# Kernel tuning notes

Measured on AMD Instinct MI355X. Metric: run time of the kernel, lower is better.

The kernel has to match this reference:

```python
import jax, jax.numpy as jnp
import numpy as np

C, N, E = 256, 256, 2048          # subgraphs, nodes/subgraph, edges/subgraph
F_IN, NHID, DDI = 128, 128, 256
K1, K2, K3 = 128, 64, 32          # top-k sizes for pooling_ratio=0.5
P, B = 16, 16                     # DAG hierarchy: P parents x B leaf children
GN = C + P + 1                    # global DAG nodes (leaves + parents + root)
GE = 8192                         # global pos/neg edge count


def setup_inputs():
    key = jax.random.key(0)
    ks = jax.random.split(key, 16)
    inp = {
        "x": jax.random.normal(ks[0], (C, N, F_IN), jnp.float32),
        "edge_index": jax.random.randint(ks[1], (C, 2, E), 0, N),
        "edge_weight": jax.random.uniform(ks[2], (C, E), dtype=jnp.float32),
        "global_edge_index": jax.random.randint(ks[3], (2, GE), 0, GN),
        "neg_edge_index": jax.random.randint(ks[4], (2, GE), 0, GN),
    }
    names = [("W1", F_IN, NHID), ("Wp1", NHID, 1), ("W2", NHID, NHID),
             ("Wp2", NHID, 1), ("W3", NHID, NHID), ("Wp3", NHID, 1),
             ("Wg", 6 * NHID, DDI), ("Wl1", DDI, DDI), ("Wl2", DDI, DDI)]
    for i, (nm, fi, fo) in enumerate(names):
        inp[nm] = jax.random.normal(ks[5 + i], (fi, fo), jnp.float32) / np.sqrt(fi)
        inp["b" + nm[1:]] = jnp.zeros((fo,), jnp.float32)
    return inp


def gcn(x, ei, ew, W, b):
    """PyG GCNConv with self-loops: D^-1/2 (A+I) D^-1/2 X W + b."""
    n = x.shape[0]
    h = x @ W
    row, col = ei[0], ei[1]
    deg = 1.0 + jax.ops.segment_sum(ew, col, num_segments=n)
    dis = jax.lax.rsqrt(deg)
    norm = dis[row] * ew * dis[col]                       # [E]
    agg = jax.ops.segment_sum(norm[:, None] * h[row], col, num_segments=n)
    return agg + h / deg[:, None] + b


def sag_pool(x, ei, ew, Ws, bs, k):
    """SAGPooling: GCN score, per-graph top-k, gate by tanh(score), edge filter."""
    n = x.shape[0]
    score = gcn(x, ei, ew, Ws, bs)[:, 0]
    vals, perm = jax.lax.top_k(score, k)
    x_new = x[perm] * jnp.tanh(vals)[:, None]
    newid = jnp.full((n,), -1, jnp.int32).at[perm].set(jnp.arange(k, dtype=jnp.int32))
    r, c = newid[ei[0]], newid[ei[1]]
    keep = (r >= 0) & (c >= 0)
    ei_new = jnp.where(keep, jnp.stack([r, c]), 0)        # dropped edges -> node 0
    ew_new = jnp.where(keep, ew, 0.0)                     # with zero weight
    return x_new, ei_new, ew_new


def _subgraph(x, ei, ew, W1, b1, Wp1, bp1, W2, b2, Wp2, bp2, W3, b3, Wp3, bp3):
    x = jax.nn.relu(gcn(x, ei, ew, W1, b1))
    x, ei, ew = sag_pool(x, ei, ew, Wp1, bp1, K1)
    x1 = jnp.concatenate([x.max(0), x.mean(0)])           # gmp||gap, batch all-zero
    x = jax.nn.relu(gcn(x, ei, ew, W2, b2))
    x, ei, ew = sag_pool(x, ei, ew, Wp2, bp2, K2)
    x2 = jnp.concatenate([x.max(0), x.mean(0)])
    x = jax.nn.relu(gcn(x, ei, ew, W3, b3))
    x, ei, ew = sag_pool(x, ei, ew, Wp3, bp3, K3)
    x3 = jnp.concatenate([x.max(0), x.mean(0)])
    return jnp.concatenate([x1, x2, x3])                  # [6*NHID]


def reference(x, edge_index, edge_weight, global_edge_index, neg_edge_index,
              W1, b1, Wp1, bp1, W2, b2, Wp2, bp2, W3, b3, Wp3, bp3,
              Wg, bg, Wl1, bl1, Wl2, bl2):
    # per-class subgraph pipeline, vmapped over the C subgraphs
    leaf = jax.vmap(_subgraph, in_axes=(0, 0, 0) + (None,) * 12)(
        x, edge_index, edge_weight,
        W1, b1, Wp1, bp1, W2, b2, Wp2, bp2, W3, b3, Wp3, bp3)   # [C, 6*NHID]
    # Get_Fs: mean-aggregate children features up the DAG (fixed 2-level + root)
    parent = leaf.reshape(P, B, -1).mean(axis=1)                # [P, 6*NHID]
    root = parent.mean(axis=0, keepdims=True)                   # [1, 6*NHID]
    gfeat = jnp.concatenate([leaf, parent, root], axis=0)       # [GN, 6*NHID]
    # global GCN (unit edge weights)
    gx = jax.nn.relu(gcn(gfeat, global_edge_index,
                         jnp.ones((GE,), gfeat.dtype), Wg, bg)) # [GN, DDI]
    class_embedding = gx[:C]
    # feature_split + lin1/lin2 + dot-product scores
    pos_s = gx[global_edge_index[0]] @ Wl1 + bl1
    pos_t = gx[global_edge_index[1]] @ Wl2 + bl2
    neg_s = gx[neg_edge_index[0]] @ Wl1 + bl1
    neg_t = gx[neg_edge_index[1]] @ Wl2 + bl2
    pos = jnp.sum(pos_s * pos_t, axis=1)
    neg = jnp.sum(neg_s * neg_t, axis=1)
    # BCEWithLogits: targets 1 for pos, 0 for neg
    loss = jnp.mean(jax.nn.softplus(-pos)) + jnp.mean(jax.nn.softplus(neg))
    return class_embedding, loss
```

## Files before the change

### kernel.cpp

```cpp
#include <hip/hip_runtime.h>
#include <math.h>

#define NT 1024
#define EDGES 2048
#define SENT 0xFFFF

struct SmemA {
  float xbuf[256 * 128];
  unsigned short rc[EDGES];
  float ewl[EDGES];
  unsigned short csr_row[EDGES];
  float csr_coef[EDGES];
  float degs[256];
  float diss[256];
  int   csr_off[257];
  int   csr_cnt[256];
  float hsv[256];
  float scorev[256];
  float vals[128];
  short perm[128];
  signed char newid[256];
};

__device__ __forceinline__ float4* xvec(float* xb, int row, int c4) {
  return reinterpret_cast<float4*>(xb + (row << 7) + ((c4 ^ (row & 7)) << 2));
}
__device__ __forceinline__ int xidx(int row, int col) {
  return (row << 7) + ((((col >> 2) ^ (row & 7)) << 2) | (col & 3));
}

template<int NN, int K, bool FIRST, bool REMAP>
__device__ __forceinline__ void run_stage(
    SmemA& sm,
    const float* __restrict__ xg,
    const int* __restrict__ eic,
    const float* __restrict__ ewc,
    const float* __restrict__ W,
    const float* __restrict__ b,
    const float* __restrict__ Wp,
    const float* __restrict__ bp,
    float& lmax, float& lmean)
{
  constexpr int NPT  = NN / 64;
  constexpr int Q    = NN / 64;
  constexpr int SEG  = NT / NN;
  constexpr int LEN  = NN / SEG;
  constexpr int LOG  = (NN == 256) ? 8 : (NN == 128 ? 7 : 6);
  const int tid  = threadIdx.x;
  const int lane = tid & 63;
  const int fbase = __builtin_amdgcn_readfirstlane((tid >> 6) << 3);
  const int c4b   = fbase >> 2;

  if (FIRST) {
    if (tid < NN) { sm.degs[tid] = 1.0f; sm.csr_cnt[tid] = 0; }
    __syncthreads();
    const float4* xg4 = reinterpret_cast<const float4*>(xg);
    for (int i = tid; i < 256 * 32; i += NT) {
      const float4 v = xg4[i];
      *xvec(sm.xbuf, i >> 5, i & 31) = v;
    }
    for (int e = tid; e < EDGES; e += NT) {
      const int row = eic[e], col = eic[EDGES + e];
      const float w = ewc[e];
      sm.rc[e]  = (unsigned short)((row << 8) | col);
      sm.ewl[e] = w;
      atomicAdd(&sm.degs[col], w);
      atomicAdd(&sm.csr_cnt[col], 1);
    }
    __syncthreads();
  }

  if (tid < NN) sm.diss[tid] = rsqrtf(sm.degs[tid]);
  if (tid < 64) {
    int c[Q], pre[Q];
    int tot = 0;
#pragma unroll
    for (int i = 0; i < Q; i++) { c[i] = sm.csr_cnt[tid * Q + i]; pre[i] = tot; tot += c[i]; }
    int inc = tot;
#pragma unroll
    for (int d = 1; d < 64; d <<= 1) {
      const int o = __shfl_up(inc, d, 64);
      if (tid >= d) inc += o;
    }
    const int base = inc - tot;
    if (tid == 0) sm.csr_off[0] = 0;
#pragma unroll
    for (int i = 0; i < Q; i++) {
      sm.csr_off[tid * Q + i + 1] = base + pre[i] + c[i];
      sm.csr_cnt[tid * Q + i] = 0;
    }
  }
  __syncthreads();

  if (tid < NN) { sm.hsv[tid] = 0.0f; sm.scorev[tid] = 0.0f; }
  for (int e = tid; e < EDGES; e += NT) {
    const unsigned short r = sm.rc[e];
    if (FIRST || r != SENT) {
      const int row = r >> 8, col = r & 255;
      const int p = atomicAdd(&sm.csr_cnt[col], 1);
      const int s = sm.csr_off[col] + p;
      sm.csr_row[s]  = (unsigned short)row;
      sm.csr_coef[s] = sm.diss[row] * sm.ewl[e];
    }
  }
  __syncthreads();

  float acc[NPT][8];
#pragma unroll
  for (int i = 0; i < NPT; i++)
#pragma unroll
    for (int j = 0; j < 8; j++) acc[i][j] = 0.0f;

#pragma unroll 4
  for (int k4 = 0; k4 < 32; k4++) {
    float4 xv[NPT];
#pragma unroll
    for (int i = 0; i < NPT; i++) xv[i] = *xvec(sm.xbuf, lane + (i << 6), k4);
#pragma unroll
    for (int kk = 0; kk < 4; kk++) {
      const float* wr = W + (((k4 << 2) + kk) << 7) + fbase;
      const float4 wa = *reinterpret_cast<const float4*>(wr);
      const float4 wb = *reinterpret_cast<const float4*>(wr + 4);
      const float wv[8] = {wa.x, wa.y, wa.z, wa.w, wb.x, wb.y, wb.z, wb.w};
#pragma unroll
      for (int i = 0; i < NPT; i++) {
        const float xs = (kk == 0) ? xv[i].x : (kk == 1) ? xv[i].y : (kk == 2) ? xv[i].z : xv[i].w;
#pragma unroll
        for (int j = 0; j < 8; j++) acc[i][j] = fmaf(xs, wv[j], acc[i][j]);
      }
    }
  }
  __syncthreads();

#pragma unroll
  for (int i = 0; i < NPT; i++) {
    const int v = lane + (i << 6);
    *xvec(sm.xbuf, v, c4b)     = make_float4(acc[i][0], acc[i][1], acc[i][2], acc[i][3]);
    *xvec(sm.xbuf, v, c4b + 1) = make_float4(acc[i][4], acc[i][5], acc[i][6], acc[i][7]);
  }
  __syncthreads();

  {
    const float4 ba = *reinterpret_cast<const float4*>(b + fbase);
    const float4 bb = *reinterpret_cast<const float4*>(b + fbase + 4);
    const float bv[8] = {ba.x, ba.y, ba.z, ba.w, bb.x, bb.y, bb.z, bb.w};
    const float4 wa = *reinterpret_cast<const float4*>(Wp + fbase);
    const float4 wb = *reinterpret_cast<const float4*>(Wp + fbase + 4);
    const float wv[8] = {wa.x, wa.y, wa.z, wa.w, wb.x, wb.y, wb.z, wb.w};
#pragma unroll
    for (int i = 0; i < NPT; i++) {
      const int v = lane + (i << 6);
      const int beg = sm.csr_off[v], end = sm.csr_off[v + 1];
      float ag[8] = {0.f, 0.f, 0.f, 0.f, 0.f, 0.f, 0.f, 0.f};
      float4 plo = make_float4(0.f, 0.f, 0.f, 0.f), phi = plo;
      float cf_nxt = 0.0f;
      if (beg < end) {
        const int r0 = sm.csr_row[beg];
        cf_nxt = sm.csr_coef[beg];
        plo = *xvec(sm.xbuf, r0, c4b);
        phi = *xvec(sm.xbuf, r0, c4b + 1);
      }
      for (int s = beg; s < end; ++s) {
        const float4 lo = plo, hi = phi;
        const float cf = cf_nxt;
        if (s + 1 < end) {
          const int rn = sm.csr_row[s + 1];
          cf_nxt = sm.csr_coef[s + 1];
          plo = *xvec(sm.xbuf, rn, c4b);
          phi = *xvec(sm.xbuf, rn, c4b + 1);
        }
        ag[0] = fmaf(cf, lo.x, ag[0]); ag[1] = fmaf(cf, lo.y, ag[1]);
        ag[2] = fmaf(cf, lo.z, ag[2]); ag[3] = fmaf(cf, lo.w, ag[3]);
        ag[4] = fmaf(cf, hi.x, ag[4]); ag[5] = fmaf(cf, hi.y, ag[5]);
        ag[6] = fmaf(cf, hi.z, ag[6]); ag[7] = fmaf(cf, hi.w, ag[7]);
      }
      const float dv = sm.diss[v];
      const float invd = 1.0f / sm.degs[v];
      float part = 0.0f;
#pragma unroll
      for (int j = 0; j < 8; j++) {
        acc[i][j] = fmaxf(fmaf(ag[j], dv, fmaf(acc[i][j], invd, bv[j])), 0.0f);
        part = fmaf(acc[i][j], wv[j], part);
      }
      atomicAdd(&sm.hsv[v], part);
    }
  }
  __syncthreads();

#pragma unroll
  for (int i = 0; i < NPT; i++) {
    const int v = lane + (i << 6);
    *xvec(sm.xbuf, v, c4b)     = make_float4(acc[i][0], acc[i][1], acc[i][2], acc[i][3]);
    *xvec(sm.xbuf, v, c4b + 1) = make_float4(acc[i][4], acc[i][5], acc[i][6], acc[i][7]);
  }
  for (int e = tid; e < EDGES; e += NT) {
    const unsigned short r = sm.rc[e];
    if (FIRST || r != SENT) {
      const int row = r >> 8, col = r & 255;
      atomicAdd(&sm.scorev[col], sm.diss[row] * sm.ewl[e] * sm.hsv[row]);
    }
  }
  __syncthreads();
  if (tid < NN) {
    sm.scorev[tid] = sm.scorev[tid] * sm.diss[tid] + sm.hsv[tid] / sm.degs[tid] + bp[0];
    sm.csr_cnt[tid] = 0;
  }
  __syncthreads();

  {
    const int node = tid & (NN - 1);
    const int seg  = tid >> LOG;
    const float sv = sm.scorev[node];
    int part = 0;
    const int u0 = seg * LEN;
#pragma unroll 4
    for (int u = u0; u < u0 + LEN; u++) {
      const float su = sm.scorev[u];
      part += (su > sv) || (su == sv && u < node);
    }
    if (part) atomicAdd(&sm.csr_cnt[node], part);
  }
  __syncthreads();
  if (tid < NN) {
    const int rank = sm.csr_cnt[tid];
    if (rank < K) { sm.perm[rank] = (short)tid; sm.vals[rank] = sm.scorev[tid]; sm.newid[tid] = (signed char)rank; }
    else sm.newid[tid] = -1;
    if (tid < K) { sm.degs[tid] = 1.0f; sm.csr_cnt[tid] = 0; }
  }
  __syncthreads();

  {
    constexpr int TPR = NT / K;
    constexpr int C4  = 32 / TPR;
    const int drow = tid / TPR;
    const int cc   = (tid % TPR) * C4;
    const int src  = sm.perm[drow];
    const float g  = tanhf(sm.vals[drow]);
    float4 tmp[C4];
#pragma unroll
    for (int j = 0; j < C4; j++) tmp[j] = *xvec(sm.xbuf, src, cc + j);
    __syncthreads();
#pragma unroll
    for (int j = 0; j < C4; j++) {
      tmp[j].x *= g; tmp[j].y *= g; tmp[j].z *= g; tmp[j].w *= g;
      *xvec(sm.xbuf, drow, cc + j) = tmp[j];
    }
  }
  __syncthreads();

  if (tid < 128) {
    float mx = -INFINITY, sv = 0.0f;
    for (int i = 0; i < K; i++) {
      const float v = sm.xbuf[xidx(i, tid)];
      mx = fmaxf(mx, v); sv += v;
    }
    lmax = mx;
    lmean = sv * (1.0f / K);
  }
  if (REMAP) {
    for (int e = tid; e < EDGES; e += NT) {
      const unsigned short r = sm.rc[e];
      if (FIRST || r != SENT) {
        const int r2 = sm.newid[r >> 8];
        const int c2 = sm.newid[r & 255];
        if (r2 < 0 || c2 < 0) sm.rc[e] = SENT;
        else {
          sm.rc[e] = (unsigned short)((r2 << 8) | c2);
          atomicAdd(&sm.degs[c2], sm.ewl[e]);
          atomicAdd(&sm.csr_cnt[c2], 1);
        }
      }
    }
  }
  __syncthreads();
}

__global__ __launch_bounds__(NT)
void stageA_kernel(const float* __restrict__ x0,
                   const int* __restrict__ ei, const float* __restrict__ ew,
                   const int* __restrict__ gei,
                   const float* __restrict__ W1, const float* __restrict__ b1,
                   const float* __restrict__ Wp1, const float* __restrict__ bp1,
                   const float* __restrict__ W2, const float* __restrict__ b2,
                   const float* __restrict__ Wp2, const float* __restrict__ bp2,
                   const float* __restrict__ W3, const float* __restrict__ b3,
                   const float* __restrict__ Wp3, const float* __restrict__ bp3,
                   const float* __restrict__ Wg, float* __restrict__ hG,
                   float* __restrict__ degG, int* __restrict__ goff,
                   int* __restrict__ gcsr_row, float* __restrict__ gcsr_coef,
                   float* __restrict__ lacc, int* __restrict__ lctr,
                   int* __restrict__ pctr)
{
  __shared__ SmemA sm;
  const int c = blockIdx.x;
  const int tid = threadIdx.x;

  if (c == 256) {
    int* cnt = (int*)sm.xbuf;
    int* off = cnt + 320;
    int* fc  = off + 321;
    for (int i = tid; i < 320; i += NT) cnt[i] = 0;
    if (tid < 288) fc[tid] = 0;
    __syncthreads();
    for (int e = tid; e < 8192; e += NT) atomicAdd(&cnt[gei[8192 + e]], 1);
    __syncthreads();
    if (tid < 64) {
      int cc[5], pre[5];
      int tot = 0;
#pragma unroll
      for (int i = 0; i < 5; i++) { cc[i] = cnt[tid * 5 + i]; pre[i] = tot; tot += cc[i]; }
      int inc = tot;
#pragma unroll
      for (int d = 1; d < 64; d <<= 1) {
        const int o = __shfl_up(inc, d, 64);
        if (tid >= d) inc += o;
      }
      const int base = inc - tot;
      if (tid == 0) off[0] = 0;
#pragma unroll
      for (int i = 0; i < 5; i++) off[tid * 5 + i + 1] = base + pre[i] + cc[i];
    }
    if (tid < 273) degG[tid] = 1.0f + (float)cnt[tid];
    __syncthreads();
    for (int e = tid; e < 8192; e += NT) {
      const int col = gei[8192 + e], row = gei[e];
      const int p = atomicAdd(&fc[col], 1);
      const int s = off[col] + p;
      gcsr_row[s]  = row;
      gcsr_coef[s] = rsqrtf(1.0f + (float)cnt[row]);
    }
    if (tid < 274) goff[tid] = off[tid];
    if (tid == 0) { *lacc = 0.0f; *lctr = 0; }

    if (tid == 0) {
      while (__hip_atomic_load(pctr, __ATOMIC_ACQUIRE, __HIP_MEMORY_SCOPE_AGENT) < 256)
        __builtin_amdgcn_s_sleep(8);
    }
    __syncthreads();
    __threadfence();

    float* racc = sm.hsv;
    if (tid < 256) racc[tid] = 0.0f;
    __syncthreads();
    for (int w = tid; w < 16 * 256; w += NT) {
      const int p = w >> 8, f = w & 255;
      float s = 0.f;
#pragma unroll 4
      for (int b2 = 0; b2 < 16; b2++) s += hG[(size_t)(p * 16 + b2) * 256 + f];
      hG[(size_t)(256 + p) * 256 + f] = s * (1.0f / 16.0f);
      atomicAdd(&racc[f], s * (1.0f / 256.0f));
    }
    __syncthreads();
    if (tid < 256) hG[(size_t)272 * 256 + tid] = racc[tid];
    return;
  }

  const int* eic = ei + (size_t)c * 2 * EDGES;
  const float* ewc = ew + (size_t)c * EDGES;
  const float* xgc = x0 + (size_t)c * 256 * 128;
  float l0 = 0.f, l1 = 0.f, l2 = 0.f, l3 = 0.f, l4 = 0.f, l5 = 0.f;
  run_stage<256, 128, true,  true >(sm, xgc, eic, ewc, W1, b1, Wp1, bp1, l0, l1);
  run_stage<128,  64, false, true >(sm, nullptr, nullptr, nullptr, W2, b2, Wp2, bp2, l2, l3);
  run_stage< 64,  32, false, false>(sm, nullptr, nullptr, nullptr, W3, b3, Wp3, bp3, l4, l5);

  float* leafbuf = sm.csr_coef;
  float* hGacc   = sm.degs;
  if (tid < 256) {
    if (tid < 128) {
      leafbuf[tid]       = l0; leafbuf[128 + tid] = l1;
      leafbuf[256 + tid] = l2; leafbuf[384 + tid] = l3;
      leafbuf[512 + tid] = l4; leafbuf[640 + tid] = l5;
    }
    hGacc[tid] = 0.0f;
  }
  __syncthreads();
  {
    const int f = tid & 255, q = tid >> 8;
    const float* wgq = Wg + (size_t)(q * 192) * 256 + f;
    const float* lb  = leafbuf + q * 192;
    float p0 = 0.f, p1 = 0.f, p2 = 0.f, p3 = 0.f;
    for (int i = 0; i < 192; i += 4) {
      p0 = fmaf(lb[i],     wgq[(size_t)i * 256],       p0);
      p1 = fmaf(lb[i + 1], wgq[(size_t)(i + 1) * 256], p1);
      p2 = fmaf(lb[i + 2], wgq[(size_t)(i + 2) * 256], p2);
      p3 = fmaf(lb[i + 3], wgq[(size_t)(i + 3) * 256], p3);
    }
    atomicAdd(&hGacc[f], (p0 + p1) + (p2 + p3));
  }
  __syncthreads();
  if (tid < 256) hG[(size_t)c * 256 + tid] = hGacc[tid];

  __syncthreads();
  if (tid == 0) {
    __threadfence();
    __hip_atomic_fetch_add(pctr, 1, __ATOMIC_RELEASE, __HIP_MEMORY_SCOPE_AGENT);
  }
}

__global__ __launch_bounds__(NT)
void gaggemb_k(const float* __restrict__ hG, const float* __restrict__ degG,
               const int* __restrict__ goff, const int* __restrict__ gcsr_row,
               const float* __restrict__ gcsr_coef, const float* __restrict__ bg,
               const float* __restrict__ Wl1, const float* __restrict__ bl1,
               const float* __restrict__ Wl2, const float* __restrict__ bl2,
               float* __restrict__ out_ce, float* __restrict__ A,
               float* __restrict__ B) {
  __shared__ float pacc[1024];
  __shared__ float pacc2[1024];
  __shared__ float gxr[256];
  const int v = blockIdx.x, tid = threadIdx.x;
  const int f = tid & 255, q = tid >> 8;
  const int beg = goff[v], end = goff[v + 1];
  float s = 0.f;
  for (int i = beg + q; i < end; i += 4)
    s = fmaf(gcsr_coef[i], hG[(size_t)gcsr_row[i] * 256 + f], s);
  pacc[tid] = s;
  __syncthreads();
  if (tid < 256) {
    const float dg = degG[v];
    float val = (pacc[tid] + pacc[256 + tid] + pacc[512 + tid] + pacc[768 + tid]) * rsqrtf(dg)
              + hG[(size_t)v * 256 + tid] / dg + bg[tid];
    val = fmaxf(val, 0.0f);
    gxr[tid] = val;
    if (v < 256) out_ce[(size_t)v * 256 + tid] = val;
  }
  __syncthreads();
  {
    const int k0 = q << 6;
    float a = 0.f, b2 = 0.f;
    for (int k = k0; k < k0 + 64; k++) {
      const float g = gxr[k];
      a  = fmaf(g, Wl1[(size_t)k * 256 + f], a);
      b2 = fmaf(g, Wl2[(size_t)k * 256 + f], b2);
    }
    pacc[tid] = a; pacc2[tid] = b2;
  }
  __syncthreads();
  if (tid < 256) {
    A[(size_t)v * 256 + tid] = pacc[tid] + pacc[256 + tid] + pacc[512 + tid] + pacc[768 + tid] + bl1[tid];
    B[(size_t)v * 256 + tid] = pacc2[tid] + pacc2[256 + tid] + pacc2[512 + tid] + pacc2[768 + tid] + bl2[tid];
  }
}

__global__ __launch_bounds__(256)
void loss_k(const float* __restrict__ A, const float* __restrict__ B,
            const int* __restrict__ gei, const int* __restrict__ nei,
            float* __restrict__ acc, int* __restrict__ lctr,
            float* __restrict__ out) {
  const int gw = (blockIdx.x * blockDim.x + threadIdx.x) >> 6;
  const int lane = threadIdx.x & 63;
  float lsum = 0.0f;
  for (int idx = gw; idx < 16384; idx += 512) {
    const bool ispos = idx < 8192;
    const int e = ispos ? idx : idx - 8192;
    const int* ia = ispos ? gei : nei;
    const int s = ia[e], t = ia[8192 + e];
    float p = 0.0f;
#pragma unroll
    for (int j = 0; j < 4; j++)
      p += A[(size_t)s * 256 + lane + 64 * j] * B[(size_t)t * 256 + lane + 64 * j];
#pragma unroll
    for (int off = 32; off; off >>= 1) p += __shfl_xor(p, off, 64);
    const float z = ispos ? -p : p;
    lsum += fmaxf(z, 0.0f) + log1pf(expf(-fabsf(z)));
  }
  if (lane == 0) atomicAdd(acc, lsum);
  __syncthreads();
  if (threadIdx.x == 0) {
    __threadfence();
    const int old = atomicAdd(lctr, 1);
    if (old == (int)gridDim.x - 1) {
      const float tot = atomicAdd(acc, 0.0f);
      out[65536] = tot * (1.0f / 8192.0f);
    }
  }
}

extern "C" void kernel_launch(void* const* d_in, const int* in_sizes, int n_in,
                              void* d_out, int out_size, void* d_ws, size_t ws_size,
                              hipStream_t stream) {
  const float* x   = (const float*)d_in[0];
  const int*   ei  = (const int*)d_in[1];
  const float* ew  = (const float*)d_in[2];
  const int*   gei = (const int*)d_in[3];
  const int*   nei = (const int*)d_in[4];
  const float* W1  = (const float*)d_in[5];
  const float* b1  = (const float*)d_in[6];
  const float* Wp1 = (const float*)d_in[7];
  const float* bp1 = (const float*)d_in[8];
  const float* W2  = (const float*)d_in[9];
  const float* b2  = (const float*)d_in[10];
  const float* Wp2 = (const float*)d_in[11];
  const float* bp2 = (const float*)d_in[12];
  const float* W3  = (const float*)d_in[13];
  const float* b3  = (const float*)d_in[14];
  const float* Wp3 = (const float*)d_in[15];
  const float* bp3 = (const float*)d_in[16];
  const float* Wg  = (const float*)d_in[17];
  const float* bg  = (const float*)d_in[18];
  const float* Wl1 = (const float*)d_in[19];
  const float* bl1 = (const float*)d_in[20];
  const float* Wl2 = (const float*)d_in[21];
  const float* bl2 = (const float*)d_in[22];

  float* ws       = (float*)d_ws;
  float* hG       = ws;
  float* degG     = hG + 273 * 256;
  float* Aemb     = degG + 288;
  float* Bemb     = Aemb + 273 * 256;
  float* lacc     = Bemb + 273 * 256;
  int*   lctr     = (int*)(lacc + 1);
  int*   pctr     = lctr + 1;
  int*   goff     = pctr + 1;
  int*   gcsr_row = goff + 288;
  float* gcsr_coef= (float*)(gcsr_row + 8192);
  float* out      = (float*)d_out;

  hipMemsetAsync(pctr, 0, sizeof(int), stream);
  stageA_kernel<<<257, NT, 0, stream>>>(x, ei, ew, gei, W1, b1, Wp1, bp1,
                                        W2, b2, Wp2, bp2, W3, b3, Wp3, bp3,
                                        Wg, hG, degG, goff, gcsr_row, gcsr_coef,
                                        lacc, lctr, pctr);
  gaggemb_k<<<273, NT, 0, stream>>>(hG, degG, goff, gcsr_row, gcsr_coef, bg,
                                    Wl1, bl1, Wl2, bl2, out, Aemb, Bemb);
  loss_k<<<128, 256, 0, stream>>>(Aemb, Bemb, gei, nei, lacc, lctr, out);
}
```

Baseline: 207.3 us.

## Split DAG prep into own kernel and fuse global GCN with loss via grid barrier

Removes the spin-waiting extra block from the subgraph kernel. Global CSR build and parent/root averaging move into a separate 17-block prep kernel, which spreads the parent reduction over 16 blocks and drops the host memset. The global aggregation/embedding kernel and the loss kernel are fused behind a software grid barrier across all 273 blocks, which relies on those blocks being co-resident. One __syncthreads after the per-subgraph CSR fill is also removed; this risks a race if later code reads the CSR before every thread has finished writing it.

```diff
diff --git a/kernel.cpp b/kernel.cpp
--- a/kernel.cpp
+++ b/kernel.cpp
@@ -103,7 +103,6 @@
       sm.csr_coef[s] = sm.diss[row] * sm.ewl[e];
     }
   }
-  __syncthreads();
 
   float acc[NPT][8];
 #pragma unroll
@@ -278,83 +277,18 @@
 __global__ __launch_bounds__(NT)
 void stageA_kernel(const float* __restrict__ x0,
                    const int* __restrict__ ei, const float* __restrict__ ew,
-                   const int* __restrict__ gei,
                    const float* __restrict__ W1, const float* __restrict__ b1,
                    const float* __restrict__ Wp1, const float* __restrict__ bp1,
                    const float* __restrict__ W2, const float* __restrict__ b2,
                    const float* __restrict__ Wp2, const float* __restrict__ bp2,
                    const float* __restrict__ W3, const float* __restrict__ b3,
                    const float* __restrict__ Wp3, const float* __restrict__ bp3,
-                   const float* __restrict__ Wg, float* __restrict__ hG,
-                   float* __restrict__ degG, int* __restrict__ goff,
-                   int* __restrict__ gcsr_row, float* __restrict__ gcsr_coef,
-                   float* __restrict__ lacc, int* __restrict__ lctr,
-                   int* __restrict__ pctr)
+                   const float* __restrict__ Wg, float* __restrict__ hG)
 {
   __shared__ SmemA sm;
   const int c = blockIdx.x;
   const int tid = threadIdx.x;
-
-  if (c == 256) {
-    int* cnt = (int*)sm.xbuf;
-    int* off = cnt + 320;
-    int* fc  = off + 321;
-    for (int i = tid; i < 320; i += NT) cnt[i] = 0;
-    if (tid < 288) fc[tid] = 0;
-    __syncthreads();
-    for (int e = tid; e < 8192; e += NT) atomicAdd(&cnt[gei[8192 + e]], 1);
-    __syncthreads();
-    if (tid < 64) {
-      int cc[5], pre[5];
-      int tot = 0;
-#pragma unroll
-      for (int i = 0; i < 5; i++) { cc[i] = cnt[tid * 5 + i]; pre[i] = tot; tot += cc[i]; }
-      int inc = tot;
-#pragma unroll
-      for (int d = 1; d < 64; d <<= 1) {
-        const int o = __shfl_up(inc, d, 64);
-        if (tid >= d) inc += o;
-      }
-      const int base = inc - tot;
-      if (tid == 0) off[0] = 0;
-#pragma unroll
-      for (int i = 0; i < 5; i++) off[tid * 5 + i + 1] = base + pre[i] + cc[i];
-    }
-    if (tid < 273) degG[tid] = 1.0f + (float)cnt[tid];
-    __syncthreads();
-    for (int e = tid; e < 8192; e += NT) {
-      const int col = gei[8192 + e], row = gei[e];
-      const int p = atomicAdd(&fc[col], 1);
-      const int s = off[col] + p;
-      gcsr_row[s]  = row;
-      gcsr_coef[s] = rsqrtf(1.0f + (float)cnt[row]);
-    }
-    if (tid < 274) goff[tid] = off[tid];
-    if (tid == 0) { *lacc = 0.0f; *lctr = 0; }
-
-    if (tid == 0) {
-      while (__hip_atomic_load(pctr, __ATOMIC_ACQUIRE, __HIP_MEMORY_SCOPE_AGENT) < 256)
-        __builtin_amdgcn_s_sleep(8);
-    }
-    __syncthreads();
-    __threadfence();
-
-    float* racc = sm.hsv;
-    if (tid < 256) racc[tid] = 0.0f;
-    __syncthreads();
-    for (int w = tid; w < 16 * 256; w += NT) {
-      const int p = w >> 8, f = w & 255;
-      float s = 0.f;
-#pragma unroll 4
-      for (int b2 = 0; b2 < 16; b2++) s += hG[(size_t)(p * 16 + b2) * 256 + f];
-      hG[(size_t)(256 + p) * 256 + f] = s * (1.0f / 16.0f);
-      atomicAdd(&racc[f], s * (1.0f / 256.0f));
-    }
-    __syncthreads();
-    if (tid < 256) hG[(size_t)272 * 256 + tid] = racc[tid];
-    return;
-  }
-
+  if (c == 0 && tid < 256) hG[(size_t)272 * 256 + tid] = 0.0f;
   const int* eic = ei + (size_t)c * 2 * EDGES;
   const float* ewc = ew + (size_t)c * EDGES;
   const float* xgc = x0 + (size_t)c * 256 * 128;
@@ -389,32 +323,90 @@
   }
   __syncthreads();
   if (tid < 256) hG[(size_t)c * 256 + tid] = hGacc[tid];
-
-  __syncthreads();
-  if (tid == 0) {
-    __threadfence();
-    __hip_atomic_fetch_add(pctr, 1, __ATOMIC_RELEASE, __HIP_MEMORY_SCOPE_AGENT);
-  }
 }
 
 __global__ __launch_bounds__(NT)
-void gaggemb_k(const float* __restrict__ hG, const float* __restrict__ degG,
-               const int* __restrict__ goff, const int* __restrict__ gcsr_row,
-               const float* __restrict__ gcsr_coef, const float* __restrict__ bg,
-               const float* __restrict__ Wl1, const float* __restrict__ bl1,
-               const float* __restrict__ Wl2, const float* __restrict__ bl2,
-               float* __restrict__ out_ce, float* __restrict__ A,
-               float* __restrict__ B) {
+void prep_k(float* __restrict__ hG, const int* __restrict__ gei,
+            float* __restrict__ degG, int* __restrict__ goff,
+            int* __restrict__ gcsr_row, float* __restrict__ gcsr_coef,
+            float* __restrict__ lacc, int* __restrict__ lctr,
+            int* __restrict__ arrive) {
+  const int tid = threadIdx.x;
+  if (blockIdx.x == 16) {
+    __shared__ int cnt[320];
+    __shared__ int off[321];
+    __shared__ int fc[288];
+    for (int i = tid; i < 320; i += NT) cnt[i] = 0;
+    if (tid < 288) fc[tid] = 0;
+    __syncthreads();
+    for (int e = tid; e < 8192; e += NT) atomicAdd(&cnt[gei[8192 + e]], 1);
+    __syncthreads();
+    if (tid < 64) {
+      int cc[5], pre[5];
+      int tot = 0;
+#pragma unroll
+      for (int i = 0; i < 5; i++) { cc[i] = cnt[tid * 5 + i]; pre[i] = tot; tot += cc[i]; }
+      int inc = tot;
+#pragma unroll
+      for (int d = 1; d < 64; d <<= 1) {
+        const int o = __shfl_up(inc, d, 64);
+        if (tid >= d) inc += o;
+      }
+      const int base = inc - tot;
+      if (tid == 0) off[0] = 0;
+#pragma unroll
+      for (int i = 0; i < 5; i++) off[tid * 5 + i + 1] = base + pre[i] + cc[i];
+    }
+    if (tid < 273) degG[tid] = 1.0f + (float)cnt[tid];
+    __syncthreads();
+    for (int e = tid; e < 8192; e += NT) {
+      const int col = gei[8192 + e], row = gei[e];
+      const int p = atomicAdd(&fc[col], 1);
+      const int s = off[col] + p;
+      gcsr_row[s]  = row;
+      gcsr_coef[s] = rsqrtf(1.0f + (float)cnt[row]);
+    }
+    if (tid < 274) goff[tid] = off[tid];
+    if (tid == 0) { *lacc = 0.0f; *lctr = 0; *arrive = 0; }
+    return;
+  }
+  __shared__ float pr[1024];
+  const int p = blockIdx.x;
+  const int f = tid & 255, q = tid >> 8;
+  float s = 0.f;
+  for (int b2 = q; b2 < 16; b2 += 4) s += hG[(size_t)(p * 16 + b2) * 256 + f];
+  pr[tid] = s;
+  __syncthreads();
+  if (tid < 256) {
+    const float sv = (pr[tid] + pr[256 + tid] + pr[512 + tid] + pr[768 + tid]) * (1.0f / 16.0f);
+    hG[(size_t)(256 + p) * 256 + tid] = sv;
+    atomicAdd(&hG[(size_t)272 * 256 + tid], sv * (1.0f / 16.0f));
+  }
+}
+
+__global__ __launch_bounds__(NT)
+void gagg_loss_k(const float* __restrict__ hG, const float* __restrict__ degG,
+                 const int* __restrict__ goff, const int* __restrict__ gcsr_row,
+                 const float* __restrict__ gcsr_coef, const float* __restrict__ bg,
+                 const float* __restrict__ Wl1, const float* __restrict__ bl1,
+                 const float* __restrict__ Wl2, const float* __restrict__ bl2,
+                 const int* __restrict__ gei, const int* __restrict__ nei,
+                 float* __restrict__ out_ce, float* __restrict__ A,
+                 float* __restrict__ B, int* __restrict__ arrive,
+                 float* __restrict__ lacc, int* __restrict__ lctr,
+                 float* __restrict__ out) {
   __shared__ float pacc[1024];
   __shared__ float pacc2[1024];
   __shared__ float gxr[256];
   const int v = blockIdx.x, tid = threadIdx.x;
   const int f = tid & 255, q = tid >> 8;
-  const int beg = goff[v], end = goff[v + 1];
-  float s = 0.f;
-  for (int i = beg + q; i < end; i += 4)
-    s = fmaf(gcsr_coef[i], hG[(size_t)gcsr_row[i] * 256 + f], s);
-  pacc[tid] = s;
+  {
+    const int beg = goff[v], end = goff[v + 1];
+    float s = 0.f;
+    for (int i = beg + q; i < end; i += 4)
+      s = fmaf(gcsr_coef[i], hG[(size_t)gcsr_row[i] * 256 + f], s);
+    pacc[tid] = s;
+  }
   __syncthreads();
   if (tid < 256) {
     const float dg = degG[v];
@@ -440,38 +432,46 @@
     A[(size_t)v * 256 + tid] = pacc[tid] + pacc[256 + tid] + pacc[512 + tid] + pacc[768 + tid] + bl1[tid];
     B[(size_t)v * 256 + tid] = pacc2[tid] + pacc2[256 + tid] + pacc2[512 + tid] + pacc2[768 + tid] + bl2[tid];
   }
-}
-
-__global__ __launch_bounds__(256)
-void loss_k(const float* __restrict__ A, const float* __restrict__ B,
-            const int* __restrict__ gei, const int* __restrict__ nei,
-            float* __restrict__ acc, int* __restrict__ lctr,
-            float* __restrict__ out) {
-  const int gw = (blockIdx.x * blockDim.x + threadIdx.x) >> 6;
-  const int lane = threadIdx.x & 63;
-  float lsum = 0.0f;
-  for (int idx = gw; idx < 16384; idx += 512) {
-    const bool ispos = idx < 8192;
-    const int e = ispos ? idx : idx - 8192;
-    const int* ia = ispos ? gei : nei;
-    const int s = ia[e], t = ia[8192 + e];
-    float p = 0.0f;
-#pragma unroll
-    for (int j = 0; j < 4; j++)
-      p += A[(size_t)s * 256 + lane + 64 * j] * B[(size_t)t * 256 + lane + 64 * j];
-#pragma unroll
-    for (int off = 32; off; off >>= 1) p += __shfl_xor(p, off, 64);
-    const float z = ispos ? -p : p;
-    lsum += fmaxf(z, 0.0f) + log1pf(expf(-fabsf(z)));
-  }
-  if (lane == 0) atomicAdd(acc, lsum);
-  __syncthreads();
-  if (threadIdx.x == 0) {
+  __syncthreads();
+
+  if (tid == 0) {
     __threadfence();
-    const int old = atomicAdd(lctr, 1);
-    if (old == (int)gridDim.x - 1) {
-      const float tot = atomicAdd(acc, 0.0f);
-      out[65536] = tot * (1.0f / 8192.0f);
+    __hip_atomic_fetch_add(arrive, 1, __ATOMIC_RELEASE, __HIP_MEMORY_SCOPE_AGENT);
+    while (__hip_atomic_load(arrive, __ATOMIC_ACQUIRE, __HIP_MEMORY_SCOPE_AGENT) < 273)
+      __builtin_amdgcn_s_sleep(2);
+    pacc[0] = 0.0f;
+  }
+  __syncthreads();
+  __threadfence();
+
+  {
+    const int gw = (v << 4) + (tid >> 6);
+    const int lane = tid & 63;
+    float lsum = 0.0f;
+    for (int idx = gw; idx < 16384; idx += 4368) {
+      const bool ispos = idx < 8192;
+      const int e = idx & 8191;
+      const int* ia = ispos ? gei : nei;
+      const int s2 = ia[e], t2 = ia[8192 + e];
+      float p = 0.0f;
+#pragma unroll
+      for (int m = 0; m < 4; m++)
+        p += A[(size_t)s2 * 256 + lane + (m << 6)] * B[(size_t)t2 * 256 + lane + (m << 6)];
+#pragma unroll
+      for (int off = 32; off; off >>= 1) p += __shfl_xor(p, off, 64);
+      const float z = ispos ? -p : p;
+      lsum += fmaxf(z, 0.0f) + log1pf(expf(-fabsf(z)));
+    }
+    if (lane == 0 && lsum != 0.0f) atomicAdd(&pacc[0], lsum);
+    __syncthreads();
+    if (tid == 0) {
+      atomicAdd(lacc, pacc[0]);
+      __threadfence();
+      const int old = atomicAdd(lctr, 1);
+      if (old == 272) {
+        const float tot = atomicAdd(lacc, 0.0f);
+        out[65536] = tot * (1.0f / 8192.0f);
+      }
     }
   }
 }
@@ -510,18 +510,18 @@
   float* Bemb     = Aemb + 273 * 256;
   float* lacc     = Bemb + 273 * 256;
   int*   lctr     = (int*)(lacc + 1);
-  int*   pctr     = lctr + 1;
-  int*   goff     = pctr + 1;
+  int*   arrive   = lctr + 1;
+  int*   goff     = arrive + 1;
   int*   gcsr_row = goff + 288;
   float* gcsr_coef= (float*)(gcsr_row + 8192);
   float* out      = (float*)d_out;
 
-  hipMemsetAsync(pctr, 0, sizeof(int), stream);
-  stageA_kernel<<<257, NT, 0, stream>>>(x, ei, ew, gei, W1, b1, Wp1, bp1,
+  stageA_kernel<<<256, NT, 0, stream>>>(x, ei, ew, W1, b1, Wp1, bp1,
                                         W2, b2, Wp2, bp2, W3, b3, Wp3, bp3,
-                                        Wg, hG, degG, goff, gcsr_row, gcsr_coef,
-                                        lacc, lctr, pctr);
-  gaggemb_k<<<273, NT, 0, stream>>>(hG, degG, goff, gcsr_row, gcsr_coef, bg,
-                                    Wl1, bl1, Wl2, bl2, out, Aemb, Bemb);
-  loss_k<<<128, 256, 0, stream>>>(Aemb, Bemb, gei, nei, lacc, lctr, out);
-}
+                                        Wg, hG);
+  prep_k<<<17, NT, 0, stream>>>(hG, gei, degG, goff, gcsr_row, gcsr_coef,
+                                lacc, lctr, arrive);
+  gagg_loss_k<<<273, NT, 0, stream>>>(hG, degG, goff, gcsr_row, gcsr_coef, bg,
+                                      Wl1, bl1, Wl2, bl2, gei, nei,
+                                      out, Aemb, Bemb, arrive, lacc, lctr, out);
+}
```

Measured after the change: 277.4 us. 1.34x slower.
